# Optimization experiments

Measured on AMD Instinct MI355X. Metric: run time of the kernel, lower is better.

## Reference

```python
import jax, jax.numpy as jnp
import numpy as np

# irreps_in = irreps_out = 32x0e + 16x1o ; irreps_sh = 1x0e + 1x1o
MUL0, MUL1 = 32, 16
N_NODES = 12000
N_EDGES = 120000
INV_SQRT3 = float(1.0 / np.sqrt(3.0))   # w3j(1,1,0), w3j(0,1,1), w3j(1,0,1) coefficient
SQRT2 = float(np.sqrt(2.0))             # e3nn normalize2mom constant for ReLU
# e3nn TP norms: irrep_normalization='component', path_normalization='element'.
# Each output irrep receives paths with num_elements 32 and 16 -> x = 48.
N_0E = float(1.0 / np.sqrt(48.0))       # alpha = dim(0e)/48 = 1/48
N_1O = float(np.sqrt(3.0 / 48.0))       # alpha = dim(1o)/48 = 3/48
# uvw weight blocks (mul2 = 1): (s,y0->s),(s,y0->g),(v,y1->s),(v,y1->g),(s,y1->v),(v,y0->v)
SPLITS = [MUL0 * MUL0, MUL0 * MUL1, MUL1 * MUL0, MUL1 * MUL1, MUL0 * MUL1, MUL1 * MUL1]
OFFS = np.cumsum([0] + SPLITS)
WNUM = int(OFFS[-1])  # 3072


def setup_inputs() -> dict:
    key = jax.random.key(0)
    k1, k2, k3, k4, k5 = jax.random.split(key, 5)
    x = jax.random.normal(k1, (N_NODES, MUL0 + 3 * MUL1), dtype=jnp.float32)
    edge_attr = jax.random.normal(k2, (N_EDGES, 64), dtype=jnp.float32)
    Yij = jax.random.normal(k3, (N_EDGES, 4), dtype=jnp.float32)
    edge_index = jax.random.randint(k4, (2, N_EDGES), 0, N_NODES, dtype=jnp.int64)
    w_emb = jax.random.normal(k5, (2 * MUL0 + 64, WNUM), dtype=jnp.float32)
    return {"x": x, "edge_attr": edge_attr, "Yij": Yij,
            "edge_index": edge_index, "w_emb": w_emb}


def reference(x, edge_attr, Yij, edge_index, w_emb):
    dst, src = edge_index[0], edge_index[1]
    E = edge_attr.shape[0]
    xs = x[:, :MUL0]                                   # [N, 32] scalars (0e)
    xv = x[:, MUL0:].reshape(-1, MUL1, 3)              # [N, 16, 3] vectors (1o)

    # per-edge weight MLP (single e3nn FC layer, weight scaled by 1/sqrt(fan_in))
    emb = jnp.concatenate([xs[dst], xs[src], edge_attr], axis=-1)     # [E, 128]
    w = emb @ (w_emb / np.sqrt(w_emb.shape[0]))                       # [E, 3072]
    Ws = [w[:, OFFS[i]:OFFS[i + 1]] for i in range(6)]
    W1 = Ws[0].reshape(E, MUL0, MUL0)
    W2 = Ws[1].reshape(E, MUL0, MUL1)
    W3 = Ws[2].reshape(E, MUL1, MUL0)
    W4 = Ws[3].reshape(E, MUL1, MUL1)
    W5 = Ws[4].reshape(E, MUL0, MUL1)
    W6 = Ws[5].reshape(E, MUL1, MUL1)

    # gather source features, split sh
    x1s, x1v = xs[src], xv[src]                        # [E,32], [E,16,3]
    y0, y1 = Yij[:, 0], Yij[:, 1:4]                    # [E], [E,3]

    sy0 = x1s * y0[:, None]                            # 0e x 0e paths
    vdot = jnp.einsum('euk,ek->eu', x1v, y1) * INV_SQRT3  # 1o x 1o -> 0e
    out_s = N_0E * (jnp.einsum('euw,eu->ew', W1, sy0) +
                    jnp.einsum('euw,eu->ew', W3, vdot))    # [E, 32]
    out_g = N_0E * (jnp.einsum('euw,eu->ew', W2, sy0) +
                    jnp.einsum('euw,eu->ew', W4, vdot))    # [E, 16]
    out_v = (N_1O * INV_SQRT3) * (
        jnp.einsum('euw,eu,ek->ewk', W5, x1s, y1) +
        jnp.einsum('euw,euk->ewk', W6, x1v * y0[:, None, None]))  # [E, 16, 3]

    msg = jnp.concatenate([out_s, out_g, out_v.reshape(E, MUL1 * 3)], axis=-1)  # [E, 96]

    # scatter mean onto destination nodes
    summed = jax.ops.segment_sum(msg, dst, num_segments=N_NODES)
    cnt = jax.ops.segment_sum(jnp.ones((E,), msg.dtype), dst, num_segments=N_NODES)
    mean = summed / jnp.maximum(cnt, 1.0)[:, None]

    # Gate (e3nn Activation normalizes ReLU by sqrt(2))
    s = SQRT2 * jax.nn.relu(mean[:, :MUL0])
    g = SQRT2 * jax.nn.relu(mean[:, MUL0:MUL0 + MUL1])
    v = mean[:, MUL0 + MUL1:].reshape(-1, MUL1, 3) * g[:, :, None]
    out = jnp.concatenate([s, v.reshape(-1, MUL1 * 3)], axis=-1)     # [N, 80]
    return x + out
```

## Files before the change

kernel.cpp:

```cpp
#include <hip/hip_runtime.h>
#include <hip/hip_bf16.h>

#define E_EDGES 120000
#define NUM_NODES 12000

typedef __attribute__((ext_vector_type(8))) short bfrag;
typedef __attribute__((ext_vector_type(8))) unsigned short ushort8;
typedef __attribute__((ext_vector_type(4))) float f32x4;

#define INV_SQRT3 0.57735026918962576f
#define SQRT2_C   1.41421356237309515f
#define N_0E_C    0.14433756729740643f
#define NV_C      0.14433756729740643f
#define WSCALE    0.08838834764831845f

__device__ __forceinline__ unsigned short f2bf(float f) {
    union { float f; unsigned int u; } v; v.f = f;
    unsigned int r = v.u + 0x7fffu + ((v.u >> 16) & 1u);
    return (unsigned short)(r >> 16);
}

__device__ __forceinline__ ushort8 pack8(f32x4 a, f32x4 b) {
    ushort8 o;
    o[0] = f2bf(a.x); o[1] = f2bf(a.y); o[2] = f2bf(a.z); o[3] = f2bf(a.w);
    o[4] = f2bf(b.x); o[5] = f2bf(b.y); o[6] = f2bf(b.z); o[7] = f2bf(b.w);
    return o;
}

__global__ void k_wt(const float* __restrict__ w_emb, unsigned short* __restrict__ Bt) {
    int o = blockIdx.x * 256 + threadIdx.x;
    if (o >= 3072 * 128) return;
    int t = o >> 11;
    int c = (o >> 3) & 255;
    int j = o & 7;
    int kb = c >> 6;
    int quad = (c >> 4) & 3;
    int col = c & 15;
    int k = kb * 32 + quad * 8 + j;
    int n = t * 16 + col;
    Bt[o] = f2bf(w_emb[k * 3072 + n] * WSCALE);
}

__global__ void k_prep(const float* __restrict__ x, const float* __restrict__ edge_attr,
                       const float* __restrict__ Yij, const int* __restrict__ edge_index,
                       unsigned short* __restrict__ emb, float* __restrict__ rT,
                       float* __restrict__ cnt) {
    int e = blockIdx.x * 256 + threadIdx.x;
    if (e >= E_EDGES) return;
    int dst = edge_index[e];
    int src = edge_index[E_EDGES + e];
    f32x4 y = *(const f32x4*)(Yij + 4 * (long)e);
    float y0 = y.x, y1a = y.y, y1b = y.z, y1c = y.w;
    const float* xd = x + (long)dst * 80;
    const float* xs = x + (long)src * 80;
    const float* ea = edge_attr + (long)e * 64;

    ushort8* embp = (ushort8*)(emb + (long)e * 128);

    float xsv[80];
#pragma unroll
    for (int i = 0; i < 80; i += 4) {
        f32x4 v = *(const f32x4*)(xs + i);
        xsv[i] = v.x; xsv[i + 1] = v.y; xsv[i + 2] = v.z; xsv[i + 3] = v.w;
    }
#pragma unroll
    for (int cb = 0; cb < 4; ++cb) {
        f32x4 a = *(const f32x4*)(xd + cb * 8);
        f32x4 b = *(const f32x4*)(xd + cb * 8 + 4);
        embp[cb] = pack8(a, b);
    }
#pragma unroll
    for (int cb = 0; cb < 4; ++cb) {
        f32x4 a, b;
        a.x = xsv[cb * 8 + 0]; a.y = xsv[cb * 8 + 1]; a.z = xsv[cb * 8 + 2]; a.w = xsv[cb * 8 + 3];
        b.x = xsv[cb * 8 + 4]; b.y = xsv[cb * 8 + 5]; b.z = xsv[cb * 8 + 6]; b.w = xsv[cb * 8 + 7];
        embp[4 + cb] = pack8(a, b);
    }
#pragma unroll
    for (int cb = 0; cb < 8; ++cb) {
        f32x4 a = *(const f32x4*)(ea + cb * 8);
        f32x4 b = *(const f32x4*)(ea + cb * 8 + 4);
        embp[8 + cb] = pack8(a, b);
    }
#pragma unroll
    for (int u = 0; u < 32; ++u) rT[(long)u * E_EDGES + e] = xsv[u] * y0;
#pragma unroll
    for (int u = 0; u < 16; ++u)
        rT[(long)(32 + u) * E_EDGES + e] =
            (xsv[32 + 3 * u] * y1a + xsv[33 + 3 * u] * y1b + xsv[34 + 3 * u] * y1c) * INV_SQRT3;
#pragma unroll
    for (int u = 0; u < 32; ++u) rT[(long)(48 + u) * E_EDGES + e] = xsv[u];
#pragma unroll
    for (int j = 0; j < 48; ++j) rT[(long)(80 + j) * E_EDGES + e] = xsv[32 + j] * y0;
    atomicAdd(cnt + dst, 1.0f);
}

__global__ __launch_bounds__(256, 4) void k_gemm(
    const unsigned short* __restrict__ emb, const unsigned short* __restrict__ Bt,
    const float* __restrict__ rT, const int* __restrict__ edge_index,
    const float* __restrict__ Yij, float* __restrict__ summed) {
    const int lane = threadIdx.x & 63;
    const int wave = threadIdx.x >> 6;
    long e0 = (long)blockIdx.x * 128 + (long)wave * 32;
    const bool dup = (e0 + 32 > E_EDGES);
    if (dup) e0 = E_EDGES - 32;
    const int col = lane & 15, quad = lane >> 4;

    __shared__ __align__(16) char lds[2][16384];

    bfrag A[2][4];
#pragma unroll
    for (int s = 0; s < 2; ++s) {
        const unsigned short* ap = emb + (e0 + s * 16 + col) * 128 + quad * 8;
#pragma unroll
        for (int kb = 0; kb < 4; ++kb) A[s][kb] = *(const bfrag*)(ap + kb * 32);
    }

    auto stage = [&](int ci) {
        const char* g = (const char*)Bt + (size_t)ci * 16384 + wave * 4096 + lane * 16;
        char* l = &lds[ci & 1][wave * 4096];
#pragma unroll
        for (int j = 0; j < 4; ++j)
            __builtin_amdgcn_global_load_lds(
                (const __attribute__((address_space(1))) unsigned int*)(g + j * 1024),
                (__attribute__((address_space(3))) unsigned int*)(l + j * 1024), 16, 0, 0);
    };

    f32x4 z = {0.f, 0.f, 0.f, 0.f};
    f32x4 acc_s0[2] = {z, z}, acc_s1[2] = {z, z}, acc_g[2] = {z, z}, acc_t5[2] = {z, z};
    f32x4 acc_v[2][3] = {{z, z, z}, {z, z, z}};

    const float* rbase = rT + e0 + quad * 4;
    auto loadw = [&](int r, f32x4& a, f32x4& b) {
        const float* p = rbase + (long)r * E_EDGES;
        a = *(const f32x4*)(p);
        b = *(const f32x4*)(p + 16);
    };

    auto tile = [&](const char* lt, f32x4& c0, f32x4& c1) {
        bfrag B0 = *(const bfrag*)(lt + lane * 16);
        bfrag B1 = *(const bfrag*)(lt + lane * 16 + 1024);
        bfrag B2 = *(const bfrag*)(lt + lane * 16 + 2048);
        bfrag B3 = *(const bfrag*)(lt + lane * 16 + 3072);
        c0 = z; c1 = z;
        c0 = __builtin_amdgcn_mfma_f32_16x16x32_bf16(A[0][0], B0, c0, 0, 0, 0);
        c1 = __builtin_amdgcn_mfma_f32_16x16x32_bf16(A[1][0], B0, c1, 0, 0, 0);
        c0 = __builtin_amdgcn_mfma_f32_16x16x32_bf16(A[0][1], B1, c0, 0, 0, 0);
        c1 = __builtin_amdgcn_mfma_f32_16x16x32_bf16(A[1][1], B1, c1, 0, 0, 0);
        c0 = __builtin_amdgcn_mfma_f32_16x16x32_bf16(A[0][2], B2, c0, 0, 0, 0);
        c1 = __builtin_amdgcn_mfma_f32_16x16x32_bf16(A[1][2], B2, c1, 0, 0, 0);
        c0 = __builtin_amdgcn_mfma_f32_16x16x32_bf16(A[0][3], B3, c0, 0, 0, 0);
        c1 = __builtin_amdgcn_mfma_f32_16x16x32_bf16(A[1][3], B3, c1, 0, 0, 0);
    };

    stage(0);
    int cidx = 0;
    auto nextbuf = [&]() -> const char* {
        __syncthreads();
        if (cidx + 1 < 48) stage(cidx + 1);
        const char* b = lds[cidx & 1];
        ++cidx;
        return b;
    };

    f32x4 c0, c1;

    {
        f32x4 p0a, p0b, p1a, p1b;
        loadw(0, p0a, p0b); loadw(1, p1a, p1b);
#pragma unroll 1
        for (int j = 0; j < 16; ++j) {
            const char* buf = nextbuf();
            f32x4 w0a = p0a, w0b = p0b, w1a = p1a, w1b = p1b;
            int nr = (j < 15) ? (2 * j + 2) : 0;
            loadw(nr, p0a, p0b); loadw(nr + 1, p1a, p1b);
            tile(buf,         c0, c1); acc_s0[0] += c0 * w0a; acc_s0[1] += c1 * w0b;
            tile(buf + 4096,  c0, c1); acc_s1[0] += c0 * w0a; acc_s1[1] += c1 * w0b;
            tile(buf + 8192,  c0, c1); acc_s0[0] += c0 * w1a; acc_s0[1] += c1 * w1b;
            tile(buf + 12288, c0, c1); acc_s1[0] += c0 * w1a; acc_s1[1] += c1 * w1b;
        }
    }
    {
        f32x4 pa[4], pb[4];
#pragma unroll
        for (int i = 0; i < 4; ++i) loadw(i, pa[i], pb[i]);
#pragma unroll 1
        for (int j = 0; j < 8; ++j) {
            const char* buf = nextbuf();
            f32x4 wa[4], wb[4];
#pragma unroll
            for (int i = 0; i < 4; ++i) { wa[i] = pa[i]; wb[i] = pb[i]; }
            int nr = (j < 7) ? (4 * j + 4) : 0;
#pragma unroll
            for (int i = 0; i < 4; ++i) loadw(nr + i, pa[i], pb[i]);
#pragma unroll
            for (int i = 0; i < 4; ++i) {
                tile(buf + i * 4096, c0, c1);
                acc_g[0] += c0 * wa[i]; acc_g[1] += c1 * wb[i];
            }
        }
    }
    {
        f32x4 p0a, p0b, p1a, p1b;
        loadw(32, p0a, p0b); loadw(33, p1a, p1b);
#pragma unroll 1
        for (int j = 0; j < 8; ++j) {
            const char* buf = nextbuf();
            f32x4 w0a = p0a, w0b = p0b, w1a = p1a, w1b = p1b;
            int nr = (j < 7) ? (32 + 2 * j + 2) : 32;
            loadw(nr, p0a, p0b); loadw(nr + 1, p1a, p1b);
            tile(buf,         c0, c1); acc_s0[0] += c0 * w0a; acc_s0[1] += c1 * w0b;
            tile(buf + 4096,  c0, c1); acc_s1[0] += c0 * w0a; acc_s1[1] += c1 * w0b;
            tile(buf + 8192,  c0, c1); acc_s0[0] += c0 * w1a; acc_s0[1] += c1 * w1b;
            tile(buf + 12288, c0, c1); acc_s1[0] += c0 * w1a; acc_s1[1] += c1 * w1b;
        }
    }
    {
        f32x4 pa[4], pb[4];
#pragma unroll
        for (int i = 0; i < 4; ++i) loadw(32 + i, pa[i], pb[i]);
#pragma unroll 1
        for (int j = 0; j < 4; ++j) {
            const char* buf = nextbuf();
            f32x4 wa[4], wb[4];
#pragma unroll
            for (int i = 0; i < 4; ++i) { wa[i] = pa[i]; wb[i] = pb[i]; }
            int nr = (j < 3) ? (32 + 4 * j + 4) : 32;
#pragma unroll
            for (int i = 0; i < 4; ++i) loadw(nr + i, pa[i], pb[i]);
#pragma unroll
            for (int i = 0; i < 4; ++i) {
                tile(buf + i * 4096, c0, c1);
                acc_g[0] += c0 * wa[i]; acc_g[1] += c1 * wb[i];
            }
        }
    }
    {
        f32x4 pa[4], pb[4];
#pragma unroll
        for (int i = 0; i < 4; ++i) loadw(48 + i, pa[i], pb[i]);
#pragma unroll 1
        for (int j = 0; j < 8; ++j) {
            const char* buf = nextbuf();
            f32x4 wa[4], wb[4];
#pragma unroll
            for (int i = 0; i < 4; ++i) { wa[i] = pa[i]; wb[i] = pb[i]; }
            int nr = (j < 7) ? (48 + 4 * j + 4) : 48;
#pragma unroll
            for (int i = 0; i < 4; ++i) loadw(nr + i, pa[i], pb[i]);
#pragma unroll
            for (int i = 0; i < 4; ++i) {
                tile(buf + i * 4096, c0, c1);
                acc_t5[0] += c0 * wa[i]; acc_t5[1] += c1 * wb[i];
            }
        }
    }
    {
        f32x4 va[3], vb[3];
#pragma unroll
        for (int k = 0; k < 3; ++k) loadw(80 + k, va[k], vb[k]);
#pragma unroll 1
        for (int j = 0; j < 4; ++j) {
            const char* buf = nextbuf();
#pragma unroll
            for (int i = 0; i < 4; ++i) {
                f32x4 wa[3], wb[3];
#pragma unroll
                for (int k = 0; k < 3; ++k) { wa[k] = va[k]; wb[k] = vb[k]; }
                int un = 4 * j + i + 1; if (un > 15) un = 0;
#pragma unroll
                for (int k = 0; k < 3; ++k) loadw(80 + 3 * un + k, va[k], vb[k]);
                tile(buf + i * 4096, c0, c1);
#pragma unroll
                for (int k = 0; k < 3; ++k) {
                    acc_v[0][k] += c0 * wa[k];
                    acc_v[1][k] += c1 * wb[k];
                }
            }
        }
    }

    if (dup) return;
#pragma unroll
    for (int s = 0; s < 2; ++s) {
        long eb = e0 + s * 16 + quad * 4;
#pragma unroll
        for (int r = 0; r < 4; ++r) {
            long e = eb + r;
            int d = edge_index[e];
            float* base = summed + (long)d * 96;
            float y1a = Yij[4 * e + 1], y1b = Yij[4 * e + 2], y1c = Yij[4 * e + 3];
            atomicAdd(base + col,       N_0E_C * acc_s0[s][r]);
            atomicAdd(base + col + 16,  N_0E_C * acc_s1[s][r]);
            atomicAdd(base + 32 + col,  N_0E_C * acc_g[s][r]);
            float t5 = acc_t5[s][r];
            atomicAdd(base + 48 + col * 3 + 0, NV_C * (t5 * y1a + acc_v[s][0][r]));
            atomicAdd(base + 48 + col * 3 + 1, NV_C * (t5 * y1b + acc_v[s][1][r]));
            atomicAdd(base + 48 + col * 3 + 2, NV_C * (t5 * y1c + acc_v[s][2][r]));
        }
    }
}

__global__ void k_final(const float* __restrict__ x, const float* __restrict__ summed,
                        const float* __restrict__ cnt, float* __restrict__ out) {
    int tid = blockIdx.x * 256 + threadIdx.x;
    if (tid >= NUM_NODES * 80) return;
    int n = tid / 80, c = tid % 80;
    float m = fmaxf(cnt[n], 1.0f);
    float inv = 1.0f / m;
    float val;
    if (c < 32) {
        val = SQRT2_C * fmaxf(summed[(long)n * 96 + c] * inv, 0.0f);
    } else {
        int j = c - 32;
        int w = j / 3;
        float g = SQRT2_C * fmaxf(summed[(long)n * 96 + 32 + w] * inv, 0.0f);
        val = summed[(long)n * 96 + 48 + j] * inv * g;
    }
    out[tid] = x[tid] + val;
}

extern "C" void kernel_launch(void* const* d_in, const int* in_sizes, int n_in,
                              void* d_out, int out_size, void* d_ws, size_t ws_size,
                              hipStream_t stream) {
    const float* x         = (const float*)d_in[0];
    const float* edge_attr = (const float*)d_in[1];
    const float* Yij       = (const float*)d_in[2];
    const int*   edge_index= (const int*)d_in[3];
    const float* w_emb     = (const float*)d_in[4];
    float* out = (float*)d_out;

    char* ws = (char*)d_ws;
    size_t off = 0;
    unsigned short* emb = (unsigned short*)(ws + off); off += (size_t)E_EDGES * 128 * 2;
    unsigned short* Bt  = (unsigned short*)(ws + off); off += (size_t)3072 * 128 * 2;
    off = (off + 255) & ~(size_t)255;
    float* rT     = (float*)(ws + off); off += (size_t)128 * E_EDGES * 4;
    size_t zoff = off;
    float* summed = (float*)(ws + off); off += (size_t)NUM_NODES * 96 * 4;
    float* cnt    = (float*)(ws + off); off += (size_t)NUM_NODES * 4;

    hipMemsetAsync(ws + zoff, 0, (size_t)NUM_NODES * 97 * 4, stream);
    k_wt  <<<(3072 * 128 + 255) / 256, 256, 0, stream>>>(w_emb, Bt);
    k_prep<<<(E_EDGES + 255) / 256, 256, 0, stream>>>(x, edge_attr, Yij, edge_index, emb, rT, cnt);
    k_gemm<<<(E_EDGES + 127) / 128, 256, 0, stream>>>(emb, Bt, rT, edge_index, Yij, summed);
    k_final<<<(NUM_NODES * 80 + 255) / 256, 256, 0, stream>>>(x, summed, cnt, out);
}
```

Before: 291.8 us.

## Split edge GEMM across two blocks per edge tile by output group

Each 128-edge tile is now handled by two blocks. One block computes the scalar output paths (W1/W3 chunks), and the other computes the gate and vector paths (W2/W4/W5/W6 chunks), each with its own chunk staging sequence. This doubles the grid and lowers the accumulator registers each block holds, which should raise parallelism and occupancy. In exchange, the A fragments (emb rows) are loaded twice and there are two kernel tails per tile.

```diff
diff --git a/kernel.cpp b/kernel.cpp
--- a/kernel.cpp
+++ b/kernel.cpp
@@ -101,7 +101,8 @@
     const float* __restrict__ Yij, float* __restrict__ summed) {
     const int lane = threadIdx.x & 63;
     const int wave = threadIdx.x >> 6;
-    long e0 = (long)blockIdx.x * 128 + (long)wave * 32;
+    const int phase = blockIdx.x & 1;
+    long e0 = (long)(blockIdx.x >> 1) * 128 + (long)wave * 32;
     const bool dup = (e0 + 32 > E_EDGES);
     if (dup) e0 = E_EDGES - 32;
     const int col = lane & 15, quad = lane >> 4;
@@ -127,8 +128,6 @@
     };
 
     f32x4 z = {0.f, 0.f, 0.f, 0.f};
-    f32x4 acc_s0[2] = {z, z}, acc_s1[2] = {z, z}, acc_g[2] = {z, z}, acc_t5[2] = {z, z};
-    f32x4 acc_v[2][3] = {{z, z, z}, {z, z, z}};
 
     const float* rbase = rT + e0 + quad * 4;
     auto loadw = [&](int r, f32x4& a, f32x4& b) {
@@ -153,150 +152,166 @@
         c1 = __builtin_amdgcn_mfma_f32_16x16x32_bf16(A[1][3], B3, c1, 0, 0, 0);
     };
 
-    stage(0);
-    int cidx = 0;
-    auto nextbuf = [&]() -> const char* {
+    int bufp = 0;
+    auto nextbuf = [&](int nxt) -> const char* {
         __syncthreads();
-        if (cidx + 1 < 48) stage(cidx + 1);
-        const char* b = lds[cidx & 1];
-        ++cidx;
+        if (nxt >= 0) stage(nxt);
+        const char* b = lds[bufp & 1];
+        ++bufp;
         return b;
     };
 
     f32x4 c0, c1;
 
-    {
-        f32x4 p0a, p0b, p1a, p1b;
-        loadw(0, p0a, p0b); loadw(1, p1a, p1b);
-#pragma unroll 1
-        for (int j = 0; j < 16; ++j) {
-            const char* buf = nextbuf();
-            f32x4 w0a = p0a, w0b = p0b, w1a = p1a, w1b = p1b;
-            int nr = (j < 15) ? (2 * j + 2) : 0;
-            loadw(nr, p0a, p0b); loadw(nr + 1, p1a, p1b);
-            tile(buf,         c0, c1); acc_s0[0] += c0 * w0a; acc_s0[1] += c1 * w0b;
-            tile(buf + 4096,  c0, c1); acc_s1[0] += c0 * w0a; acc_s1[1] += c1 * w0b;
-            tile(buf + 8192,  c0, c1); acc_s0[0] += c0 * w1a; acc_s0[1] += c1 * w1b;
-            tile(buf + 12288, c0, c1); acc_s1[0] += c0 * w1a; acc_s1[1] += c1 * w1b;
-        }
-    }
-    {
-        f32x4 pa[4], pb[4];
-#pragma unroll
-        for (int i = 0; i < 4; ++i) loadw(i, pa[i], pb[i]);
-#pragma unroll 1
-        for (int j = 0; j < 8; ++j) {
-            const char* buf = nextbuf();
-            f32x4 wa[4], wb[4];
-#pragma unroll
-            for (int i = 0; i < 4; ++i) { wa[i] = pa[i]; wb[i] = pb[i]; }
-            int nr = (j < 7) ? (4 * j + 4) : 0;
-#pragma unroll
-            for (int i = 0; i < 4; ++i) loadw(nr + i, pa[i], pb[i]);
-#pragma unroll
-            for (int i = 0; i < 4; ++i) {
-                tile(buf + i * 4096, c0, c1);
-                acc_g[0] += c0 * wa[i]; acc_g[1] += c1 * wb[i];
-            }
-        }
-    }
-    {
-        f32x4 p0a, p0b, p1a, p1b;
-        loadw(32, p0a, p0b); loadw(33, p1a, p1b);
-#pragma unroll 1
-        for (int j = 0; j < 8; ++j) {
-            const char* buf = nextbuf();
-            f32x4 w0a = p0a, w0b = p0b, w1a = p1a, w1b = p1b;
-            int nr = (j < 7) ? (32 + 2 * j + 2) : 32;
-            loadw(nr, p0a, p0b); loadw(nr + 1, p1a, p1b);
-            tile(buf,         c0, c1); acc_s0[0] += c0 * w0a; acc_s0[1] += c1 * w0b;
-            tile(buf + 4096,  c0, c1); acc_s1[0] += c0 * w0a; acc_s1[1] += c1 * w0b;
-            tile(buf + 8192,  c0, c1); acc_s0[0] += c0 * w1a; acc_s0[1] += c1 * w1b;
-            tile(buf + 12288, c0, c1); acc_s1[0] += c0 * w1a; acc_s1[1] += c1 * w1b;
-        }
-    }
-    {
-        f32x4 pa[4], pb[4];
-#pragma unroll
-        for (int i = 0; i < 4; ++i) loadw(32 + i, pa[i], pb[i]);
-#pragma unroll 1
-        for (int j = 0; j < 4; ++j) {
-            const char* buf = nextbuf();
-            f32x4 wa[4], wb[4];
-#pragma unroll
-            for (int i = 0; i < 4; ++i) { wa[i] = pa[i]; wb[i] = pb[i]; }
-            int nr = (j < 3) ? (32 + 4 * j + 4) : 32;
-#pragma unroll
-            for (int i = 0; i < 4; ++i) loadw(nr + i, pa[i], pb[i]);
-#pragma unroll
-            for (int i = 0; i < 4; ++i) {
-                tile(buf + i * 4096, c0, c1);
-                acc_g[0] += c0 * wa[i]; acc_g[1] += c1 * wb[i];
-            }
-        }
-    }
-    {
-        f32x4 pa[4], pb[4];
-#pragma unroll
-        for (int i = 0; i < 4; ++i) loadw(48 + i, pa[i], pb[i]);
-#pragma unroll 1
-        for (int j = 0; j < 8; ++j) {
-            const char* buf = nextbuf();
-            f32x4 wa[4], wb[4];
-#pragma unroll
-            for (int i = 0; i < 4; ++i) { wa[i] = pa[i]; wb[i] = pb[i]; }
-            int nr = (j < 7) ? (48 + 4 * j + 4) : 48;
-#pragma unroll
-            for (int i = 0; i < 4; ++i) loadw(nr + i, pa[i], pb[i]);
-#pragma unroll
-            for (int i = 0; i < 4; ++i) {
-                tile(buf + i * 4096, c0, c1);
-                acc_t5[0] += c0 * wa[i]; acc_t5[1] += c1 * wb[i];
-            }
-        }
-    }
-    {
-        f32x4 va[3], vb[3];
-#pragma unroll
-        for (int k = 0; k < 3; ++k) loadw(80 + k, va[k], vb[k]);
-#pragma unroll 1
-        for (int j = 0; j < 4; ++j) {
-            const char* buf = nextbuf();
-#pragma unroll
-            for (int i = 0; i < 4; ++i) {
-                f32x4 wa[3], wb[3];
-#pragma unroll
-                for (int k = 0; k < 3; ++k) { wa[k] = va[k]; wb[k] = vb[k]; }
-                int un = 4 * j + i + 1; if (un > 15) un = 0;
-#pragma unroll
-                for (int k = 0; k < 3; ++k) loadw(80 + 3 * un + k, va[k], vb[k]);
-                tile(buf + i * 4096, c0, c1);
-#pragma unroll
-                for (int k = 0; k < 3; ++k) {
-                    acc_v[0][k] += c0 * wa[k];
-                    acc_v[1][k] += c1 * wb[k];
+    if (phase == 0) {
+        f32x4 acc_s0[2] = {z, z}, acc_s1[2] = {z, z};
+        stage(0);
+        {
+            f32x4 p0a, p0b, p1a, p1b;
+            loadw(0, p0a, p0b); loadw(1, p1a, p1b);
+#pragma unroll 1
+            for (int j = 0; j < 16; ++j) {
+                const char* buf = nextbuf(j < 15 ? j + 1 : 24);
+                f32x4 w0a = p0a, w0b = p0b, w1a = p1a, w1b = p1b;
+                int nr = (j < 15) ? (2 * j + 2) : 32;
+                loadw(nr, p0a, p0b); loadw(nr + 1, p1a, p1b);
+                tile(buf,         c0, c1); acc_s0[0] += c0 * w0a; acc_s0[1] += c1 * w0b;
+                tile(buf + 4096,  c0, c1); acc_s1[0] += c0 * w0a; acc_s1[1] += c1 * w0b;
+                tile(buf + 8192,  c0, c1); acc_s0[0] += c0 * w1a; acc_s0[1] += c1 * w1b;
+                tile(buf + 12288, c0, c1); acc_s1[0] += c0 * w1a; acc_s1[1] += c1 * w1b;
+            }
+        }
+        {
+            f32x4 p0a, p0b, p1a, p1b;
+            loadw(32, p0a, p0b); loadw(33, p1a, p1b);
+#pragma unroll 1
+            for (int j = 0; j < 8; ++j) {
+                const char* buf = nextbuf(j < 7 ? 25 + j : -1);
+                f32x4 w0a = p0a, w0b = p0b, w1a = p1a, w1b = p1b;
+                int nr = (j < 7) ? (32 + 2 * j + 2) : 32;
+                loadw(nr, p0a, p0b); loadw(nr + 1, p1a, p1b);
+                tile(buf,         c0, c1); acc_s0[0] += c0 * w0a; acc_s0[1] += c1 * w0b;
+                tile(buf + 4096,  c0, c1); acc_s1[0] += c0 * w0a; acc_s1[1] += c1 * w0b;
+                tile(buf + 8192,  c0, c1); acc_s0[0] += c0 * w1a; acc_s0[1] += c1 * w1b;
+                tile(buf + 12288, c0, c1); acc_s1[0] += c0 * w1a; acc_s1[1] += c1 * w1b;
+            }
+        }
+        if (dup) return;
+#pragma unroll
+        for (int s = 0; s < 2; ++s) {
+            long eb = e0 + s * 16 + quad * 4;
+#pragma unroll
+            for (int r = 0; r < 4; ++r) {
+                int d = edge_index[eb + r];
+                float* base = summed + (long)d * 96;
+                atomicAdd(base + col,      N_0E_C * acc_s0[s][r]);
+                atomicAdd(base + col + 16, N_0E_C * acc_s1[s][r]);
+            }
+        }
+    } else {
+        f32x4 acc_g[2] = {z, z}, acc_t5[2] = {z, z};
+        f32x4 acc_v[2][3] = {{z, z, z}, {z, z, z}};
+        stage(16);
+        {
+            f32x4 pa[4], pb[4];
+#pragma unroll
+            for (int i = 0; i < 4; ++i) loadw(i, pa[i], pb[i]);
+#pragma unroll 1
+            for (int j = 0; j < 8; ++j) {
+                const char* buf = nextbuf(j < 7 ? 17 + j : 32);
+                f32x4 wa[4], wb[4];
+#pragma unroll
+                for (int i = 0; i < 4; ++i) { wa[i] = pa[i]; wb[i] = pb[i]; }
+                int nr = (j < 7) ? (4 * j + 4) : 32;
+#pragma unroll
+                for (int i = 0; i < 4; ++i) loadw(nr + i, pa[i], pb[i]);
+#pragma unroll
+                for (int i = 0; i < 4; ++i) {
+                    tile(buf + i * 4096, c0, c1);
+                    acc_g[0] += c0 * wa[i]; acc_g[1] += c1 * wb[i];
                 }
             }
         }
-    }
-
-    if (dup) return;
-#pragma unroll
-    for (int s = 0; s < 2; ++s) {
-        long eb = e0 + s * 16 + quad * 4;
-#pragma unroll
-        for (int r = 0; r < 4; ++r) {
-            long e = eb + r;
-            int d = edge_index[e];
-            float* base = summed + (long)d * 96;
-            float y1a = Yij[4 * e + 1], y1b = Yij[4 * e + 2], y1c = Yij[4 * e + 3];
-            atomicAdd(base + col,       N_0E_C * acc_s0[s][r]);
-            atomicAdd(base + col + 16,  N_0E_C * acc_s1[s][r]);
-            atomicAdd(base + 32 + col,  N_0E_C * acc_g[s][r]);
-            float t5 = acc_t5[s][r];
-            atomicAdd(base + 48 + col * 3 + 0, NV_C * (t5 * y1a + acc_v[s][0][r]));
-            atomicAdd(base + 48 + col * 3 + 1, NV_C * (t5 * y1b + acc_v[s][1][r]));
-            atomicAdd(base + 48 + col * 3 + 2, NV_C * (t5 * y1c + acc_v[s][2][r]));
+        {
+            f32x4 pa[4], pb[4];
+#pragma unroll
+            for (int i = 0; i < 4; ++i) loadw(32 + i, pa[i], pb[i]);
+#pragma unroll 1
+            for (int j = 0; j < 4; ++j) {
+                const char* buf = nextbuf(33 + j);
+                f32x4 wa[4], wb[4];
+#pragma unroll
+                for (int i = 0; i < 4; ++i) { wa[i] = pa[i]; wb[i] = pb[i]; }
+                int nr = (j < 3) ? (32 + 4 * j + 4) : 48;
+#pragma unroll
+                for (int i = 0; i < 4; ++i) loadw(nr + i, pa[i], pb[i]);
+#pragma unroll
+                for (int i = 0; i < 4; ++i) {
+                    tile(buf + i * 4096, c0, c1);
+                    acc_g[0] += c0 * wa[i]; acc_g[1] += c1 * wb[i];
+                }
+            }
+        }
+        {
+            f32x4 pa[4], pb[4];
+#pragma unroll
+            for (int i = 0; i < 4; ++i) loadw(48 + i, pa[i], pb[i]);
+#pragma unroll 1
+            for (int j = 0; j < 8; ++j) {
+                const char* buf = nextbuf(37 + j);
+                f32x4 wa[4], wb[4];
+#pragma unroll
+                for (int i = 0; i < 4; ++i) { wa[i] = pa[i]; wb[i] = pb[i]; }
+                int nr = (j < 7) ? (48 + 4 * j + 4) : 48;
+#pragma unroll
+                for (int i = 0; i < 4; ++i) loadw(nr + i, pa[i], pb[i]);
+#pragma unroll
+                for (int i = 0; i < 4; ++i) {
+                    tile(buf + i * 4096, c0, c1);
+                    acc_t5[0] += c0 * wa[i]; acc_t5[1] += c1 * wb[i];
+                }
+            }
+        }
+        {
+            f32x4 va[3], vb[3];
+#pragma unroll
+            for (int k = 0; k < 3; ++k) loadw(80 + k, va[k], vb[k]);
+#pragma unroll 1
+            for (int j = 0; j < 4; ++j) {
+                const char* buf = nextbuf(j < 3 ? 45 + j : -1);
+#pragma unroll
+                for (int i = 0; i < 4; ++i) {
+                    f32x4 wa[3], wb[3];
+#pragma unroll
+                    for (int k = 0; k < 3; ++k) { wa[k] = va[k]; wb[k] = vb[k]; }
+                    int un = 4 * j + i + 1; if (un > 15) un = 0;
+#pragma unroll
+                    for (int k = 0; k < 3; ++k) loadw(80 + 3 * un + k, va[k], vb[k]);
+                    tile(buf + i * 4096, c0, c1);
+#pragma unroll
+                    for (int k = 0; k < 3; ++k) {
+                        acc_v[0][k] += c0 * wa[k];
+                        acc_v[1][k] += c1 * wb[k];
+                    }
+                }
+            }
+        }
+        if (dup) return;
+#pragma unroll
+        for (int s = 0; s < 2; ++s) {
+            long eb = e0 + s * 16 + quad * 4;
+#pragma unroll
+            for (int r = 0; r < 4; ++r) {
+                long e = eb + r;
+                int d = edge_index[e];
+                float* base = summed + (long)d * 96;
+                float y1a = Yij[4 * e + 1], y1b = Yij[4 * e + 2], y1c = Yij[4 * e + 3];
+                atomicAdd(base + 32 + col, N_0E_C * acc_g[s][r]);
+                float t5 = acc_t5[s][r];
+                atomicAdd(base + 48 + col * 3 + 0, NV_C * (t5 * y1a + acc_v[s][0][r]));
+                atomicAdd(base + 48 + col * 3 + 1, NV_C * (t5 * y1b + acc_v[s][1][r]));
+                atomicAdd(base + 48 + col * 3 + 2, NV_C * (t5 * y1c + acc_v[s][2][r]));
+            }
         }
     }
 }
@@ -343,6 +358,6 @@
     hipMemsetAsync(ws + zoff, 0, (size_t)NUM_NODES * 97 * 4, stream);
     k_wt  <<<(3072 * 128 + 255) / 256, 256, 0, stream>>>(w_emb, Bt);
     k_prep<<<(E_EDGES + 255) / 256, 256, 0, stream>>>(x, edge_attr, Yij, edge_index, emb, rT, cnt);
-    k_gemm<<<(E_EDGES + 127) / 128, 256, 0, stream>>>(emb, Bt, rT, edge_index, Yij, summed);
+    k_gemm<<<2 * ((E_EDGES + 127) / 128), 256, 0, stream>>>(emb, Bt, rT, edge_index, Yij, summed);
     k_final<<<(NUM_NODES * 80 + 255) / 256, 256, 0, stream>>>(x, summed, cnt, out);
 }
```

After: 293.8 us. Within noise of the previous version (+0.7%).
